# Optimization experiments

Hardware: AMD Instinct MI355X
Metric: run time of the kernel (lower is better)

Reference implementation:

```python
import jax, jax.numpy as jnp
import numpy as np

B, S, D, H, F = 16, 512, 768, 12, 3072
E = 4      # unique sequence-level experts
M = 4      # inner SwitchFeedForward experts
SW = 128   # switch encoder dim
EPS = 1e-12


def setup_inputs() -> dict:
    key = jax.random.key(0)
    ks = iter(jax.random.split(key, 64))
    def p(shape):
        return jax.random.normal(next(ks), shape, jnp.float32) * 0.02
    inp = {}
    inp['hidden_states'] = jax.random.normal(next(ks), (B, S, D), jnp.float32)
    inp['attention_mask'] = jnp.zeros((B, S), jnp.float32)
    inp['cluster_list'] = jnp.zeros((B,), jnp.int32)
    # router
    inp['sw_enc_w'] = p((D, SW)); inp['sw_enc_b'] = jnp.zeros((SW,), jnp.float32)
    inp['sw_w'] = p((SW, E));     inp['sw_b'] = jnp.zeros((E,), jnp.float32)
    # common attention
    for n in ('q', 'k', 'v', 'o'):
        inp['ca_w' + n] = p((D, D)); inp['ca_b' + n] = jnp.zeros((D,), jnp.float32)
    # unique attentions (stacked over E experts)
    for n in ('q', 'k', 'v', 'o'):
        inp['ua_w' + n] = p((E, D, D)); inp['ua_b' + n] = jnp.zeros((E, D), jnp.float32)
    # common FFN (plain GELU MLP)
    inp['cf_w1'] = p((D, F)); inp['cf_b1'] = jnp.zeros((F,), jnp.float32)
    inp['cf_w2'] = p((F, D)); inp['cf_b2'] = jnp.zeros((D,), jnp.float32)
    # unique FFNs: each is a top-1 SwitchFeedForward with M inner experts
    inp['uf_sw_w'] = p((E, D, M)); inp['uf_sw_b'] = jnp.zeros((E, M), jnp.float32)
    inp['uf_w1'] = p((E, M, D, F)); inp['uf_b1'] = jnp.zeros((E, M, F), jnp.float32)
    inp['uf_w2'] = p((E, M, F, D)); inp['uf_b2'] = jnp.zeros((E, M, D), jnp.float32)
    # output LayerNorm
    inp['ln_g'] = jnp.ones((D,), jnp.float32); inp['ln_b'] = jnp.zeros((D,), jnp.float32)
    return inp


def _attn(x, mask, wq, bq, wk, bk, wv, bv, wo, bo):
    b, s, d = x.shape
    dh = d // H
    q = (x @ wq + bq).reshape(b, s, H, dh)
    k = (x @ wk + bk).reshape(b, s, H, dh)
    v = (x @ wv + bv).reshape(b, s, H, dh)
    sc = jnp.einsum('bqhd,bkhd->bhqk', q, k) / jnp.sqrt(jnp.float32(dh))
    sc = sc + mask[:, None, None, :]
    pr = jax.nn.softmax(sc, axis=-1)
    o = jnp.einsum('bhqk,bkhd->bqhd', pr, v).reshape(b, s, d)
    return o @ wo + bo


def _switch_ffn(x, sww, swb, w1, b1, w2, b2):
    # top-1 token routing over M inner experts, output scaled by route_prob_max
    rp = jax.nn.softmax(x @ sww + swb, axis=-1)            # [b,s,M]
    gate = jax.nn.one_hot(jnp.argmax(rp, -1), M) * jnp.max(rp, -1, keepdims=True)
    h = jax.nn.gelu(jnp.einsum('bsd,mdf->bsmf', x, w1) + b1, approximate=False)
    y = jnp.einsum('bsmf,mfd->bsmd', h, w2) + b2
    return jnp.einsum('bsm,bsmd->bsd', gate, y)


def _forward(hidden_states, attention_mask, sw_enc_w, sw_enc_b, sw_w, sw_b,
             ca_wq, ca_bq, ca_wk, ca_bk, ca_wv, ca_bv, ca_wo, ca_bo,
             ua_wq, ua_bq, ua_wk, ua_bk, ua_wv, ua_bv, ua_wo, ua_bo,
             cf_w1, cf_b1, cf_w2, cf_b2,
             uf_sw_w, uf_sw_b, uf_w1, uf_b1, uf_w2, uf_b2, ln_g, ln_b):
    # sequence-level router: softmax over pooled hidden states, top-1 expert
    pooled = hidden_states.mean(axis=1)                    # [B,D]
    rp = jax.nn.softmax((pooled @ sw_enc_w + sw_enc_b) @ sw_w + sw_b, axis=-1)
    pm = jnp.max(rp, axis=-1)                              # [B]
    sel = jax.nn.one_hot(jnp.argmax(rp, axis=-1), E)       # [B,E]

    common_attn = _attn(hidden_states, attention_mask,
                        ca_wq, ca_bq, ca_wk, ca_bk, ca_wv, ca_bv, ca_wo, ca_bo)
    unique_attn = jnp.zeros_like(hidden_states)
    for i in range(E):
        oi = _attn(hidden_states, attention_mask,
                   ua_wq[i], ua_bq[i], ua_wk[i], ua_bk[i],
                   ua_wv[i], ua_bv[i], ua_wo[i], ua_bo[i])
        unique_attn = unique_attn + sel[:, i, None, None] * oi
    unique_attn = unique_attn * pm[:, None, None]          # scale by route prob
    att_output = common_attn + unique_attn

    unique_ffn = jnp.zeros_like(hidden_states)
    for i in range(E):
        yi = _switch_ffn(att_output, uf_sw_w[i], uf_sw_b[i],
                         uf_w1[i], uf_b1[i], uf_w2[i], uf_b2[i])
        unique_ffn = unique_ffn + sel[:, i, None, None] * yi
    common_ffn = jax.nn.gelu(att_output @ cf_w1 + cf_b1, approximate=False) @ cf_w2 + cf_b2
    ffn_output = common_ffn + unique_ffn                   # dropout is identity (eval)

    x = att_output + ffn_output
    mu = x.mean(-1, keepdims=True)
    var = jnp.mean((x - mu) ** 2, -1, keepdims=True)
    return (x - mu) / jnp.sqrt(var + EPS) * ln_g + ln_b


def reference(hidden_states, attention_mask, cluster_list, sw_enc_w, sw_enc_b, sw_w, sw_b,
              ca_wq, ca_bq, ca_wk, ca_bk, ca_wv, ca_bv, ca_wo, ca_bo,
              ua_wq, ua_bq, ua_wk, ua_bk, ua_wv, ua_bv, ua_wo, ua_bo,
              cf_w1, cf_b1, cf_w2, cf_b2,
              uf_sw_w, uf_sw_b, uf_w1, uf_b1, uf_w2, uf_b2, ln_g, ln_b):
    # cluster_list is only used in the warm-up branch; warm_up_step=0 -> ignored
    return _forward(hidden_states, attention_mask, sw_enc_w, sw_enc_b, sw_w, sw_b,
                    ca_wq, ca_bq, ca_wk, ca_bk, ca_wv, ca_bv, ca_wo, ca_bo,
                    ua_wq, ua_bq, ua_wk, ua_bk, ua_wv, ua_bv, ua_wo, ua_bo,
                    cf_w1, cf_b1, cf_w2, cf_b2,
                    uf_sw_w, uf_sw_b, uf_w1, uf_b1, uf_w2, uf_b2, ln_g, ln_b)
```

## Files before the change

kernel.cpp:

```cpp
#include <hip/hip_runtime.h>
#include <cstdint>
#include <cstddef>

#define Bq  16
#define Sq  512
#define Dq  768
#define Hq  12
#define DHq 64
#define Fq  3072
#define SWq 128
#define NTq 8192

typedef float        f32x4  __attribute__((ext_vector_type(4)));
typedef float        f32x16 __attribute__((ext_vector_type(16)));
typedef unsigned int u32x4  __attribute__((ext_vector_type(4)));
typedef __bf16       bf16x8 __attribute__((ext_vector_type(8)));
typedef _Float16     f16x8  __attribute__((ext_vector_type(8)));
typedef _Float16     f16x4  __attribute__((ext_vector_type(4)));
typedef _Float16     f16x2  __attribute__((ext_vector_type(2)));
typedef int          i32x2  __attribute__((ext_vector_type(2)));

__device__ __forceinline__ unsigned short f2bf(float f){
  unsigned int u = __builtin_bit_cast(unsigned int, f);
  u = (u + 0x7fffu + ((u >> 16) & 1u)) >> 16;
  return (unsigned short)u;
}
__device__ __forceinline__ unsigned int pk2(float a, float b){
  return (unsigned int)f2bf(a) | ((unsigned int)f2bf(b) << 16);
}
__device__ __forceinline__ i32x2 pl32swap(unsigned int a, unsigned int b){
  return __builtin_amdgcn_permlane32_swap((int)a, (int)b, false, false);
}
__device__ __forceinline__ f16x2 cvt_pk(float a, float b){
  return __builtin_bit_cast(f16x2, __builtin_amdgcn_cvt_pkrtz(a, b));
}

typedef __attribute__((address_space(1))) void vg_t;
typedef __attribute__((address_space(3))) void vl_t;
__device__ __forceinline__ void gl_lds16(const void* g, void* l){
  __builtin_amdgcn_global_load_lds((vg_t*)g, (vl_t*)l, 16, 0, 0);
}

__device__ __forceinline__ void swz2d(int &bx, int &by){
  const int gx = gridDim.x, gy = gridDim.y;
  const int nb = gx * gy;
  const int bid = blockIdx.y * gx + blockIdx.x;
  if (((nb & 7) == 0) && ((gy & 7) == 0)){
    const int chunk = nb >> 3;
    const int lb = (bid & 7) * chunk + (bid >> 3);
    const int bw = gx << 3;
    const int band = lb / bw;
    const int wn = lb - band * bw;
    bx = wn >> 3;
    by = (band << 3) + (wn & 7);
  } else {
    bx = blockIdx.x; by = blockIdx.y;
  }
}

__global__ void pooled_partial_k(const float* __restrict__ x, float* __restrict__ part){
  const int b = blockIdx.x, dc = blockIdx.y, z = blockIdx.z;
  const int d = dc*256 + threadIdx.x;
  const float* p = x + (size_t)b*Sq*Dq + (size_t)z*128*Dq + d;
  float s = 0.f;
  #pragma unroll 4
  for (int i = 0; i < 128; i++) s += p[(size_t)i*Dq];
  part[((size_t)z*Bq + b)*Dq + d] = s;
}

__global__ void router_seq_k(const float* __restrict__ part,
    const float* __restrict__ ew, const float* __restrict__ eb,
    const float* __restrict__ sw, const float* __restrict__ sb,
    int* __restrict__ sel, float* __restrict__ pm)
{
  const int b = blockIdx.x, j = threadIdx.x;
  __shared__ float h[SWq];
  __shared__ float pl[Dq];
  #pragma unroll
  for (int i = 0; i < 6; i++){
    int d = j + i*128;
    float s = part[(size_t)(0*Bq+b)*Dq + d] + part[(size_t)(1*Bq+b)*Dq + d]
            + part[(size_t)(2*Bq+b)*Dq + d] + part[(size_t)(3*Bq+b)*Dq + d];
    pl[d] = s * (1.0f/512.0f);
  }
  __syncthreads();
  float a = eb[j];
  for (int d = 0; d < Dq; d++) a += pl[d] * ew[d*SWq + j];
  h[j] = a;
  __syncthreads();
  if (j == 0){
    float lg[4];
    for (int e = 0; e < 4; e++){
      float t = sb[e];
      for (int k = 0; k < SWq; k++) t += h[k] * sw[k*4 + e];
      lg[e] = t;
    }
    float mx = fmaxf(fmaxf(lg[0],lg[1]), fmaxf(lg[2],lg[3]));
    float p[4], ssum = 0.f;
    for (int e = 0; e < 4; e++){ p[e] = expf(lg[e]-mx); ssum += p[e]; }
    int am = 0; float bv = p[0];
    for (int e = 1; e < 4; e++) if (p[e] > bv){ bv = p[e]; am = e; }
    sel[b] = am; pm[b] = bv/ssum;
  }
}

__global__ void split_f16_k(const float* __restrict__ x, _Float16* __restrict__ hh,
                            _Float16* __restrict__ ll, int n4){
  const int i = blockIdx.x*256 + threadIdx.x;
  if (i >= n4) return;
  f32x4 v = ((const f32x4*)x)[i];
  f16x4 vh, vl;
  #pragma unroll
  for (int j = 0; j < 4; j++){
    float s = v[j] * 1024.0f;
    _Float16 a = (_Float16)s;
    vh[j] = a;
    vl[j] = (_Float16)(s - (float)a);
  }
  ((f16x4*)hh)[i] = vh;
  ((f16x4*)ll)[i] = vl;
}

__global__ void transpose_f16s_k(const float* __restrict__ src,
    _Float16* __restrict__ dH, _Float16* __restrict__ dL,
    int K, int N, long srcStride, long dstStride, int rowOff)
{
  __shared__ float t[64][65];
  const int tid = threadIdx.x;
  const size_t so = (size_t)blockIdx.z * srcStride;
  const size_t dof = (size_t)blockIdx.z * dstStride;
  const int k0 = blockIdx.y * 64, n0 = blockIdx.x * 64;
  const int r = tid >> 2, c0 = (tid & 3) * 16;
  const float* sp = src + so + (size_t)(k0 + r) * N + n0 + c0;
  #pragma unroll
  for (int cc = 0; cc < 16; cc += 4){
    f32x4 v = *(const f32x4*)(sp + cc);
    t[r][c0+cc] = v[0]; t[r][c0+cc+1] = v[1]; t[r][c0+cc+2] = v[2]; t[r][c0+cc+3] = v[3];
  }
  __syncthreads();
  _Float16* ph = dH + dof + (size_t)(rowOff + n0 + r) * K + k0 + c0;
  _Float16* pl = dL + dof + (size_t)(rowOff + n0 + r) * K + k0 + c0;
  #pragma unroll
  for (int cc = 0; cc < 16; cc += 4){
    f16x4 vh, vl;
    #pragma unroll
    for (int j = 0; j < 4; j++){
      float s = t[c0+cc+j][r] * 1024.0f;
      _Float16 a = (_Float16)s;
      vh[j] = a; vl[j] = (_Float16)(s - (float)a);
    }
    *(f16x4*)(ph + cc) = vh;
    *(f16x4*)(pl + cc) = vl;
  }
}

__global__ void concat_bias3_k(const float* __restrict__ bq, const float* __restrict__ bk,
    const float* __restrict__ bv, float* __restrict__ dst, int srcStride)
{
  const int e = blockIdx.y;
  const int i = blockIdx.x*256 + threadIdx.x;
  dst[(size_t)e*2304 + i]        = bq[(size_t)e*srcStride + i];
  dst[(size_t)e*2304 + 768 + i]  = bk[(size_t)e*srcStride + i];
  dst[(size_t)e*2304 + 1536 + i] = bv[(size_t)e*srcStride + i];
}

template<int BMODE, int OMODE>
__global__ __launch_bounds__(256,2) void gemm_f16s_k(
    const _Float16* __restrict__ AH, const _Float16* __restrict__ AL,
    const _Float16* __restrict__ BH, const _Float16* __restrict__ BL,
    const float* __restrict__ bias, float* __restrict__ C,
    _Float16* __restrict__ Ch, _Float16* __restrict__ Cl,
    int N, int K, long estride, int bias_stride,
    const int* __restrict__ sel, const float* __restrict__ pm)
{
  __shared__ _Float16 AsH[128][32];
  __shared__ _Float16 AsL[128][32];
  __shared__ _Float16 BsH[128][32];
  __shared__ _Float16 BsL[128][32];
  const int tid = threadIdx.x;
  const int lane = tid & 63, wave = tid >> 6;
  const int wm = wave >> 1, wn = wave & 1;
  int bx, by; swz2d(bx, by);
  const int row0 = by * 128, col0 = bx * 128;
  const _Float16* bh = BH; const _Float16* bl = BL; const float* bp = bias;
  float cs = 1.0f;
  if constexpr (BMODE == 1){
    const int e = sel[row0 >> 9];
    bh += (size_t)e * estride; bl += (size_t)e * estride;
    bp += (size_t)e * bias_stride;
  }
  if constexpr (OMODE == 1) cs = pm[row0 >> 9];

  const int lr = lane >> 2, lk = (lane & 3) * 8;
  const _Float16 *pAH[2], *pAL[2], *pBH[2], *pBL[2];
  _Float16 *lAH[2], *lAL[2], *lBH[2], *lBL[2];
  #pragma unroll
  for (int j = 0; j < 2; j++){
    const int ia = wave*2 + j;
    pAH[j] = AH + (size_t)(row0 + ia*16 + lr)*K + lk;
    pAL[j] = AL + (size_t)(row0 + ia*16 + lr)*K + lk;
    pBH[j] = bh + (size_t)(col0 + ia*16 + lr)*K + lk;
    pBL[j] = bl + (size_t)(col0 + ia*16 + lr)*K + lk;
    lAH[j] = &AsH[0][0] + ia*512;
    lAL[j] = &AsL[0][0] + ia*512;
    lBH[j] = &BsH[0][0] + ia*512;
    lBL[j] = &BsL[0][0] + ia*512;
  }

  f32x4 acc[4][4];
  #pragma unroll
  for (int mi=0;mi<4;mi++)
    #pragma unroll
    for (int ni=0;ni<4;ni++) acc[mi][ni] = (f32x4){0.f,0.f,0.f,0.f};

  for (int k0 = 0; k0 < K; k0 += 32){
    __syncthreads();
    #pragma unroll
    for (int j = 0; j < 2; j++){
      gl_lds16(pAH[j] + k0, lAH[j]);
      gl_lds16(pAL[j] + k0, lAL[j]);
      gl_lds16(pBH[j] + k0, lBH[j]);
      gl_lds16(pBL[j] + k0, lBL[j]);
    }
    __syncthreads();
    f16x8 fah[4], fal[4], fbh[4], fbl[4];
    #pragma unroll
    for (int mi=0;mi<4;mi++){
      const int r = wm*64 + mi*16 + (lane&15), c = 8*(lane>>4);
      fah[mi] = __builtin_bit_cast(f16x8, *(const u32x4*)&AsH[r][c]);
      fal[mi] = __builtin_bit_cast(f16x8, *(const u32x4*)&AsL[r][c]);
    }
    #pragma unroll
    for (int ni=0;ni<4;ni++){
      const int r = wn*64 + ni*16 + (lane&15), c = 8*(lane>>4);
      fbh[ni] = __builtin_bit_cast(f16x8, *(const u32x4*)&BsH[r][c]);
      fbl[ni] = __builtin_bit_cast(f16x8, *(const u32x4*)&BsL[r][c]);
    }
    #pragma unroll
    for (int mi=0;mi<4;mi++)
      #pragma unroll
      for (int ni=0;ni<4;ni++){
        acc[mi][ni] = __builtin_amdgcn_mfma_f32_16x16x32_f16(fah[mi], fbh[ni], acc[mi][ni], 0, 0, 0);
        acc[mi][ni] = __builtin_amdgcn_mfma_f32_16x16x32_f16(fah[mi], fbl[ni], acc[mi][ni], 0, 0, 0);
        acc[mi][ni] = __builtin_amdgcn_mfma_f32_16x16x32_f16(fal[mi], fbh[ni], acc[mi][ni], 0, 0, 0);
      }
  }

  const float INV = 1.0f/1048576.0f;
  const int erow = 4*(lane >> 4);
  const int ecol = lane & 15;
  #pragma unroll
  for (int mi=0;mi<4;mi++)
    #pragma unroll
    for (int ni=0;ni<4;ni++){
      const int c = col0 + wn*64 + ni*16 + ecol;
      const float bb = bp[c];
      #pragma unroll
      for (int r=0;r<4;r++){
        const int R = row0 + wm*64 + mi*16 + erow + r;
        const float v = acc[mi][ni][r]*INV + bb;
        if constexpr (OMODE == 0){
          C[(size_t)R*N + c] = v;
        } else if constexpr (OMODE == 1){
          C[(size_t)R*N + c] += cs*v;
        } else {
          const float vs = v * 1024.0f;
          const _Float16 hi = (_Float16)vs;
          Ch[(size_t)R*N + c] = hi;
          Cl[(size_t)R*N + c] = (_Float16)(vs - (float)hi);
        }
      }
    }
}

__global__ __launch_bounds__(256,2) void attn_mfma_k(
    const _Float16* __restrict__ qkvH, const _Float16* __restrict__ qkvL,
    const float* __restrict__ mask,
    _Float16* __restrict__ ctxH, _Float16* __restrict__ ctxL)
{
  __shared__ _Float16 Kh[64][72], Kl[64][72];
  __shared__ _Float16 Vh[64][72], Vl[64][72];
  __shared__ float msk[64];
  __shared__ float rsi[4][32];
  const int qb = blockIdx.x, h = blockIdx.y, b = blockIdx.z;
  const int tid = threadIdx.x;
  const int l = tid & 63, w = tid >> 6;
  const int l31 = l & 31, g5 = l >> 5;
  const float SC = 1.0f/8388608.0f;

  u32x4 qfh[4], qfl[4];
  {
    const size_t qoff = (size_t)(b*Sq + qb*128 + w*32 + l31) * 2304 + h*DHq + g5*8;
    #pragma unroll
    for (int c = 0; c < 4; c++){
      qfh[c] = *(const u32x4*)(qkvH + qoff + c*16);
      qfl[c] = *(const u32x4*)(qkvL + qoff + c*16);
    }
  }
  f32x16 oacc[2];
  #pragma unroll
  for (int nt = 0; nt < 2; nt++)
    #pragma unroll
    for (int i = 0; i < 16; i++) oacc[nt][i] = 0.f;
  float rsl = 0.f;
  const float* mrow = mask + b*Sq;

  for (int kt = 0; kt < 8; kt++){
    __syncthreads();
    {
      const size_t krow = (size_t)(b*Sq + kt*64 + l) * 2304 + 768 + h*DHq;
      #pragma unroll
      for (int i = 0; i < 2; i++){
        const int ch = w + i*4;
        *(u32x4*)&Kh[l][ch*8] = *(const u32x4*)(qkvH + krow + ch*8);
        *(u32x4*)&Kl[l][ch*8] = *(const u32x4*)(qkvL + krow + ch*8);
      }
      const size_t vrow = krow + 768 + w*16;
      f16x8 v0 = __builtin_bit_cast(f16x8, *(const u32x4*)(qkvH + vrow));
      f16x8 v1 = __builtin_bit_cast(f16x8, *(const u32x4*)(qkvH + vrow + 8));
      f16x8 u0 = __builtin_bit_cast(f16x8, *(const u32x4*)(qkvL + vrow));
      f16x8 u1 = __builtin_bit_cast(f16x8, *(const u32x4*)(qkvL + vrow + 8));
      #pragma unroll
      for (int i = 0; i < 8; i++){
        Vh[w*16 + i][l] = v0[i]; Vh[w*16 + 8 + i][l] = v1[i];
        Vl[w*16 + i][l] = u0[i]; Vl[w*16 + 8 + i][l] = u1[i];
      }
      if (tid < 64) msk[tid] = mrow[kt*64 + tid] + 6.9314718055994531f;
    }
    __syncthreads();

    f32x16 sacc[2];
    #pragma unroll
    for (int mt = 0; mt < 2; mt++)
      #pragma unroll
      for (int i = 0; i < 16; i++) sacc[mt][i] = 0.f;
    #pragma unroll
    for (int mt = 0; mt < 2; mt++){
      #pragma unroll
      for (int c = 0; c < 4; c++){
        f16x8 kh = __builtin_bit_cast(f16x8, *(const u32x4*)&Kh[mt*32 + l31][c*16 + g5*8]);
        f16x8 kl = __builtin_bit_cast(f16x8, *(const u32x4*)&Kl[mt*32 + l31][c*16 + g5*8]);
        f16x8 qh = __builtin_bit_cast(f16x8, qfh[c]);
        f16x8 ql = __builtin_bit_cast(f16x8, qfl[c]);
        sacc[mt] = __builtin_amdgcn_mfma_f32_32x32x16_f16(kh, qh, sacc[mt], 0, 0, 0);
        sacc[mt] = __builtin_amdgcn_mfma_f32_32x32x16_f16(kh, ql, sacc[mt], 0, 0, 0);
        sacc[mt] = __builtin_amdgcn_mfma_f32_32x32x16_f16(kl, qh, sacc[mt], 0, 0, 0);
      }
    }

    unsigned int hP[2][4][2], lP[2][4][2];
    #pragma unroll
    for (int mt = 0; mt < 2; mt++){
      #pragma unroll
      for (int m = 0; m < 4; m++){
        f32x4 mk = *(const f32x4*)&msk[mt*32 + m*8 + g5*4];
        float p0 = __expf(fmaf(sacc[mt][4*m+0], SC, mk[0]));
        float p1 = __expf(fmaf(sacc[mt][4*m+1], SC, mk[1]));
        float p2 = __expf(fmaf(sacc[mt][4*m+2], SC, mk[2]));
        float p3 = __expf(fmaf(sacc[mt][4*m+3], SC, mk[3]));
        rsl += (p0 + p1) + (p2 + p3);
        f16x2 h0 = cvt_pk(p0, p1);
        f16x2 h1 = cvt_pk(p2, p3);
        f16x2 e0, e1;
        e0[0] = (_Float16)(p0 - (float)h0[0]); e0[1] = (_Float16)(p1 - (float)h0[1]);
        e1[0] = (_Float16)(p2 - (float)h1[0]); e1[1] = (_Float16)(p3 - (float)h1[1]);
        hP[mt][m][0] = __builtin_bit_cast(unsigned int, h0);
        hP[mt][m][1] = __builtin_bit_cast(unsigned int, h1);
        lP[mt][m][0] = __builtin_bit_cast(unsigned int, e0);
        lP[mt][m][1] = __builtin_bit_cast(unsigned int, e1);
      }
    }

    #pragma unroll
    for (int mt = 0; mt < 2; mt++){
      #pragma unroll
      for (int cc = 0; cc < 2; cc++){
        i32x2 sh0 = pl32swap(hP[mt][2*cc][0], hP[mt][2*cc+1][0]);
        i32x2 sh1 = pl32swap(hP[mt][2*cc][1], hP[mt][2*cc+1][1]);
        i32x2 sl0 = pl32swap(lP[mt][2*cc][0], lP[mt][2*cc+1][0]);
        i32x2 sl1 = pl32swap(lP[mt][2*cc][1], lP[mt][2*cc+1][1]);
        u32x4 pah = (u32x4){(unsigned)sh0[0], (unsigned)sh1[0], (unsigned)sh0[1], (unsigned)sh1[1]};
        u32x4 pal = (u32x4){(unsigned)sl0[0], (unsigned)sl1[0], (unsigned)sl0[1], (unsigned)sl1[1]};
        f16x8 ph = __builtin_bit_cast(f16x8, pah);
        f16x8 pe = __builtin_bit_cast(f16x8, pal);
        const int kof = (mt*2 + cc)*16 + g5*8;
        #pragma unroll
        for (int nt = 0; nt < 2; nt++){
          f16x8 vh = __builtin_bit_cast(f16x8, *(const u32x4*)&Vh[nt*32 + l31][kof]);
          f16x8 vl = __builtin_bit_cast(f16x8, *(const u32x4*)&Vl[nt*32 + l31][kof]);
          oacc[nt] = __builtin_amdgcn_mfma_f32_32x32x16_f16(ph, vh, oacc[nt], 0, 0, 0);
          oacc[nt] = __builtin_amdgcn_mfma_f32_32x32x16_f16(ph, vl, oacc[nt], 0, 0, 0);
          oacc[nt] = __builtin_amdgcn_mfma_f32_32x32x16_f16(pe, vh, oacc[nt], 0, 0, 0);
        }
      }
    }
  }

  {
    unsigned int rb = __builtin_bit_cast(unsigned int, rsl);
    i32x2 sw = pl32swap(rb, rb);
    float partner = __builtin_bit_cast(float, (l >= 32) ? sw[0] : sw[1]);
    float tot = rsl + partner;
    if (l < 32) rsi[w][l31] = 1.0f / tot;
  }
  __syncthreads();

  const size_t obase = (size_t)(b*Sq + qb*128 + w*32);
  #pragma unroll
  for (int nt = 0; nt < 2; nt++){
    const int col = h*DHq + nt*32 + l31;
    #pragma unroll
    for (int r = 0; r < 16; r++){
      const int q = (r&3) + 8*(r>>2) + 4*g5;
      const float v = oacc[nt][r] * rsi[w][q];
      const _Float16 hi = (_Float16)v;
      const size_t off = (obase + q)*Dq + col;
      ctxH[off] = hi;
      ctxL[off] = (_Float16)(v - (float)hi);
    }
  }
}

__global__ void transpose_bf16_k(const float* __restrict__ src, unsigned short* __restrict__ dst,
                                 int K, int N)
{
  __shared__ float t[64][65];
  const int tid = threadIdx.x;
  const size_t mo = (size_t)blockIdx.z * K * N;
  const int k0 = blockIdx.y * 64, n0 = blockIdx.x * 64;
  const int r = tid >> 2, c0 = (tid & 3) * 16;
  const float* sp = src + mo + (size_t)(k0 + r) * N + n0 + c0;
  #pragma unroll
  for (int cc = 0; cc < 16; cc += 4){
    f32x4 v = *(const f32x4*)(sp + cc);
    t[r][c0+cc] = v[0]; t[r][c0+cc+1] = v[1]; t[r][c0+cc+2] = v[2]; t[r][c0+cc+3] = v[3];
  }
  __syncthreads();
  unsigned short* dp = dst + mo + (size_t)(n0 + r) * K + k0 + c0;
  u32x4 h0, h1v;
  #pragma unroll
  for (int i = 0; i < 4; i++) h0[i]  = pk2(t[c0+2*i  ][r], t[c0+2*i+1][r]);
  #pragma unroll
  for (int i = 0; i < 4; i++) h1v[i] = pk2(t[c0+8+2*i][r], t[c0+9+2*i][r]);
  *(u32x4*)(dp)     = h0;
  *(u32x4*)(dp + 8) = h1v;
}

template<int MT, int AMODE, int OMODE, bool GELU_, bool GROUPED>
__global__ __launch_bounds__(256,2) void gemm_bf16_k(
    const void* __restrict__ Av, const unsigned short* __restrict__ BT,
    const float* __restrict__ bias, float* __restrict__ Cf, unsigned short* __restrict__ Cb,
    int N, int K,
    const int* __restrict__ tile_g, const int* __restrict__ tile_r0,
    const int* __restrict__ grp_off, const int* __restrict__ n_tiles,
    const int* __restrict__ tok_idx, const float* __restrict__ gate_s,
    size_t bstride, int bias_stride)
{
  constexpr int MI = MT / 32;
  constexpr int AI = MT / 64;
  __shared__ unsigned short As[MT][32];
  __shared__ unsigned short Bs[128][32];
  const int tid = threadIdx.x;
  const int lane = tid & 63, wave = tid >> 6;
  const int wm = wave >> 1, wn = wave & 1;
  int col0, row0, gend = 1 << 30, g = 0;
  if constexpr (GROUPED){
    const int gx = gridDim.x;
    const int nb = gx * gridDim.y;
    const int bid = blockIdx.y * gx + blockIdx.x;
    int lb = bid;
    if ((nb & 7) == 0) lb = (bid & 7) * (nb >> 3) + (bid >> 3);
    const int t = lb / gx;
    col0 = (lb - t * gx) * 128;
    if (t >= *n_tiles) return;
    g = tile_g[t];
    row0 = grp_off[g] + tile_r0[t];
    gend = grp_off[g+1];
  } else {
    int bx, by; swz2d(bx, by);
    row0 = by * MT;
    col0 = bx * 128;
  }
  const unsigned short* Bp = BT + (size_t)g * bstride;
  const float* bp = bias + (size_t)g * bias_stride;

  const int lr = lane >> 2, lk8 = (lane & 3) * 8;
  const unsigned short* pB[2]; unsigned short* lB[2];
  #pragma unroll
  for (int j = 0; j < 2; j++){
    const int ib = wave*2 + j;
    pB[j] = Bp + (size_t)(col0 + ib*16 + lr)*K + lk8;
    lB[j] = &Bs[0][0] + ib*512;
  }
  const unsigned short* pA2[AI]; unsigned short* lA2[AI];
  const float* afp = nullptr; int sa_r = 0, sa_k = 0;
  if constexpr (AMODE == 2){
    #pragma unroll
    for (int j = 0; j < AI; j++){
      int r = row0 + (wave*AI + j)*16 + lr;
      if constexpr (GROUPED) r = (r < gend - 1) ? r : (gend - 1);
      pA2[j] = (const unsigned short*)Av + (size_t)r*K + lk8;
      lA2[j] = &As[0][0] + (wave*AI + j)*512;
    }
  } else {
    sa_r = (MT == 128) ? (tid >> 1) : (tid >> 2);
    sa_k = (MT == 128) ? ((tid & 1) * 16) : ((tid & 3) * 8);
    int arow = row0 + sa_r;
    if constexpr (GROUPED) arow = (arow < gend - 1) ? arow : (gend - 1);
    if constexpr (AMODE == 1) arow = tok_idx[arow];
    afp = (const float*)Av + (size_t)arow * K + sa_k;
  }

  f32x4 acc[MI][4];
  #pragma unroll
  for (int mi=0;mi<MI;mi++)
    #pragma unroll
    for (int ni=0;ni<4;ni++) acc[mi][ni] = (f32x4){0.f,0.f,0.f,0.f};

  for (int k0 = 0; k0 < K; k0 += 32){
    u32x4 al0, al1;
    if constexpr (AMODE != 2){
      f32x4 f0 = *(const f32x4*)(afp + k0);
      f32x4 f1 = *(const f32x4*)(afp + k0 + 4);
      al0[0]=pk2(f0[0],f0[1]); al0[1]=pk2(f0[2],f0[3]); al0[2]=pk2(f1[0],f1[1]); al0[3]=pk2(f1[2],f1[3]);
      if constexpr (MT == 128){
        f32x4 f2 = *(const f32x4*)(afp + k0 + 8);
        f32x4 f3 = *(const f32x4*)(afp + k0 + 12);
        al1[0]=pk2(f2[0],f2[1]); al1[1]=pk2(f2[2],f2[3]); al1[2]=pk2(f3[0],f3[1]); al1[3]=pk2(f3[2],f3[3]);
      }
    }
    __syncthreads();
    if constexpr (AMODE == 2){
      #pragma unroll
      for (int j = 0; j < AI; j++) gl_lds16(pA2[j] + k0, lA2[j]);
    } else {
      *(u32x4*)&As[sa_r][sa_k] = al0;
      if constexpr (MT == 128) *(u32x4*)&As[sa_r][sa_k + 8] = al1;
    }
    gl_lds16(pB[0] + k0, lB[0]);
    gl_lds16(pB[1] + k0, lB[1]);
    __syncthreads();
    bf16x8 af[MI], bfr[4];
    #pragma unroll
    for (int mi=0;mi<MI;mi++){
      u32x4 t = *(const u32x4*)&As[wm*(MT/2) + mi*16 + (lane&15)][8*(lane>>4)];
      af[mi] = __builtin_bit_cast(bf16x8, t);
    }
    #pragma unroll
    for (int ni=0;ni<4;ni++){
      u32x4 t = *(const u32x4*)&Bs[wn*64 + ni*16 + (lane&15)][8*(lane>>4)];
      bfr[ni] = __builtin_bit_cast(bf16x8, t);
    }
    #pragma unroll
    for (int mi=0;mi<MI;mi++)
      #pragma unroll
      for (int ni=0;ni<4;ni++)
        acc[mi][ni] = __builtin_amdgcn_mfma_f32_16x16x32_bf16(af[mi], bfr[ni], acc[mi][ni], 0, 0, 0);
  }

  const int erow = 4*(lane >> 4);
  const int ecol = lane & 15;
  #pragma unroll
  for (int mi=0;mi<MI;mi++)
    #pragma unroll
    for (int ni=0;ni<4;ni++){
      const int c = col0 + wn*64 + ni*16 + ecol;
      const float bb = bp[c];
      #pragma unroll
      for (int r=0;r<4;r++){
        const int R = row0 + wm*(MT/2) + mi*16 + erow + r;
        if (GROUPED && R >= gend) continue;
        float v = acc[mi][ni][r] + bb;
        if (GELU_) v = 0.5f*v*(1.0f + erff(v*0.70710678118654752f));
        if constexpr (OMODE == 0){
          Cb[(size_t)R*N + c] = f2bf(v);
        } else if constexpr (OMODE == 1){
          Cf[(size_t)R*N + c] = v;
        } else {
          const int tok = tok_idx[R];
          const float gt = gate_s[R];
          float* p = Cf + (size_t)tok*N + c;
          *p += gt*v;
        }
      }
    }
}

__global__ void token_router_k(const float* __restrict__ att, const int* __restrict__ sel,
    const float* __restrict__ sww, const float* __restrict__ swb,
    int* __restrict__ grp, float* __restrict__ gate, int* __restrict__ grp_cnt)
{
  const int t = blockIdx.x*4 + (threadIdx.x >> 6);
  const int lane = threadIdx.x & 63;
  const int e = sel[t >> 9];
  const float* x = att + (size_t)t * Dq;
  const float* w = sww + (size_t)e * Dq * 4;
  float a0=0.f, a1=0.f, a2=0.f, a3=0.f;
  #pragma unroll 4
  for (int i = 0; i < 12; i++){
    const int d = lane + i*64;
    const float xv = x[d];
    f32x4 wv = *(const f32x4*)&w[d*4];
    a0 += xv*wv[0]; a1 += xv*wv[1]; a2 += xv*wv[2]; a3 += xv*wv[3];
  }
  #pragma unroll
  for (int off = 32; off; off >>= 1){
    a0 += __shfl_xor(a0, off); a1 += __shfl_xor(a1, off);
    a2 += __shfl_xor(a2, off); a3 += __shfl_xor(a3, off);
  }
  if (lane == 0){
    const float l0 = a0 + swb[e*4+0], l1 = a1 + swb[e*4+1];
    const float l2 = a2 + swb[e*4+2], l3 = a3 + swb[e*4+3];
    const float mx = fmaxf(fmaxf(l0,l1), fmaxf(l2,l3));
    const float p0 = expf(l0-mx), p1 = expf(l1-mx), p2 = expf(l2-mx), p3 = expf(l3-mx);
    const float ssum = p0+p1+p2+p3;
    int am = 0; float bv = p0;
    if (p1 > bv){ bv=p1; am=1; }
    if (p2 > bv){ bv=p2; am=2; }
    if (p3 > bv){ bv=p3; am=3; }
    grp[t] = e*4 + am;
    gate[t] = bv/ssum;
    atomicAdd(&grp_cnt[e*4 + am], 1);
  }
}

__global__ void build_offsets_k(const int* __restrict__ grp_cnt, int* __restrict__ grp_off,
    int* __restrict__ tg128, int* __restrict__ tr128, int* __restrict__ nt128,
    int* __restrict__ tg64, int* __restrict__ tr64, int* __restrict__ nt64)
{
  int off = 0, n1 = 0, n2 = 0;
  for (int g = 0; g < 16; g++){
    grp_off[g] = off;
    const int c = grp_cnt[g];
    for (int r0 = 0; r0 < c; r0 += 128){ tg128[n1] = g; tr128[n1] = r0; n1++; }
    for (int r0 = 0; r0 < c; r0 += 64){  tg64[n2]  = g; tr64[n2]  = r0; n2++; }
    off += c;
  }
  grp_off[16] = off;
  *nt128 = n1; *nt64 = n2;
}

__global__ void scatter_k(const int* __restrict__ grp, const float* __restrict__ gate,
    const int* __restrict__ grp_off, int* __restrict__ fill,
    int* __restrict__ tok_idx, float* __restrict__ gate_s)
{
  const int t = blockIdx.x*256 + threadIdx.x;
  const int g = grp[t];
  const int pos = grp_off[g] + atomicAdd(&fill[g], 1);
  tok_idx[pos] = t;
  gate_s[pos] = gate[t];
}

__global__ __launch_bounds__(256) void final_ln_k(const float* __restrict__ att,
    const float* __restrict__ acc, const float* __restrict__ lg,
    const float* __restrict__ lb, float* __restrict__ out)
{
  const int row = blockIdx.x, tid = threadIdx.x;
  const float* a = att + (size_t)row * Dq;
  const float* c = acc + (size_t)row * Dq;
  float x[3];
  #pragma unroll
  for (int i = 0; i < 3; i++) x[i] = a[tid + 256*i] + c[tid + 256*i];
  __shared__ float red[256];
  red[tid] = x[0] + x[1] + x[2];
  __syncthreads();
  for (int st = 128; st; st >>= 1){
    if (tid < st) red[tid] += red[tid + st];
    __syncthreads();
  }
  const float mu = red[0] * (1.0f/768.0f);
  __syncthreads();
  const float d0 = x[0]-mu, d1 = x[1]-mu, d2 = x[2]-mu;
  red[tid] = d0*d0 + d1*d1 + d2*d2;
  __syncthreads();
  for (int st = 128; st; st >>= 1){
    if (tid < st) red[tid] += red[tid + st];
    __syncthreads();
  }
  const float inv = 1.0f/sqrtf(red[0]*(1.0f/768.0f) + 1e-12f);
  #pragma unroll
  for (int i = 0; i < 3; i++){
    const int col = tid + 256*i;
    out[(size_t)row*Dq + col] = (x[i]-mu)*inv*lg[col] + lb[col];
  }
}

extern "C" void kernel_launch(void* const* d_in, const int* in_sizes, int n_in,
                              void* d_out, int out_size, void* d_ws, size_t ws_size,
                              hipStream_t stream)
{
  (void)in_sizes; (void)n_in; (void)out_size; (void)ws_size;
  const float* hs    = (const float*)d_in[0];
  const float* amask = (const float*)d_in[1];
  const float* sw_enc_w = (const float*)d_in[3];
  const float* sw_enc_b = (const float*)d_in[4];
  const float* sw_w  = (const float*)d_in[5];
  const float* sw_b  = (const float*)d_in[6];
  const float* ca_wq = (const float*)d_in[7];
  const float* ca_bq = (const float*)d_in[8];
  const float* ca_wk = (const float*)d_in[9];
  const float* ca_bk = (const float*)d_in[10];
  const float* ca_wv = (const float*)d_in[11];
  const float* ca_bv = (const float*)d_in[12];
  const float* ca_wo = (const float*)d_in[13];
  const float* ca_bo = (const float*)d_in[14];
  const float* ua_wq = (const float*)d_in[15];
  const float* ua_bq = (const float*)d_in[16];
  const float* ua_wk = (const float*)d_in[17];
  const float* ua_bk = (const float*)d_in[18];
  const float* ua_wv = (const float*)d_in[19];
  const float* ua_bv = (const float*)d_in[20];
  const float* ua_wo = (const float*)d_in[21];
  const float* ua_bo = (const float*)d_in[22];
  const float* cf_w1 = (const float*)d_in[23];
  const float* cf_b1 = (const float*)d_in[24];
  const float* cf_w2 = (const float*)d_in[25];
  const float* cf_b2 = (const float*)d_in[26];
  const float* uf_sw_w = (const float*)d_in[27];
  const float* uf_sw_b = (const float*)d_in[28];
  const float* uf_w1 = (const float*)d_in[29];
  const float* uf_b1 = (const float*)d_in[30];
  const float* uf_w2 = (const float*)d_in[31];
  const float* uf_b2 = (const float*)d_in[32];
  const float* ln_g  = (const float*)d_in[33];
  const float* ln_b  = (const float*)d_in[34];
  float* out = (float*)d_out;

  char* W = (char*)d_ws;
  int*   sel     = (int*)(W + 0);
  float* pm      = (float*)(W + 64);
  int*   grp_cnt = (int*)(W + 128);
  int*   fill    = (int*)(W + 192);
  int*   ntile   = (int*)(W + 256);
  int*   ntile64 = (int*)(W + 320);
  int*   grp_off = (int*)(W + 512);
  int*   tile_g  = (int*)(W + 1024);
  int*   tile_r  = (int*)(W + 2048);
  int*   tile_g64= (int*)(W + 3072);
  int*   tile_r64= (int*)(W + 4096);

  float* att  = (float*)(W + 8192);
  float* facc = (float*)(W + 25174016);
  const size_t X = 50339840;
  _Float16* hsH  = (_Float16*)(W + X);
  _Float16* hsL  = (_Float16*)(W + X + 12582912);
  _Float16* qkvH = (_Float16*)(W + X + 25165824);
  _Float16* qkvL = (_Float16*)(W + X + 62914560);
  _Float16* ctxH = (_Float16*)(W + X + 100663296);
  _Float16* ctxL = (_Float16*)(W + X + 113246208);
  _Float16* wqkv_cH = (_Float16*)(W + X + 125829120);
  _Float16* wqkv_cL = (_Float16*)(W + X + 129368064);
  _Float16* wqkv_uH = (_Float16*)(W + X + 132907008);
  _Float16* wqkv_uL = (_Float16*)(W + X + 147062784);
  _Float16* wo_cH   = (_Float16*)(W + X + 161218560);
  _Float16* wo_cL   = (_Float16*)(W + X + 162398208);
  _Float16* wo_uH   = (_Float16*)(W + X + 163577856);
  _Float16* wo_uL   = (_Float16*)(W + X + 168296448);
  float* qkvb_c = (float*)(W + X + 173015040);
  float* qkvb_u = (float*)(W + X + 173024256);
  float* partb  = (float*)(W + X + 173061120);

  unsigned short* w1T = (unsigned short*)(W + X);
  unsigned short* w2T = (unsigned short*)(W + X + 80216064);
  unsigned short* h1  = (unsigned short*)(W + X + 160432128);
  int*   grp     = (int*)(W + 261103616);
  float* gate    = (float*)(W + 261136384);
  int*   tok_idx = (int*)(W + 261169152);
  float* gate_s  = (float*)(W + 261201920);

  hipMemsetAsync(W, 0, 512, stream);

  pooled_partial_k<<<dim3(Bq,3,4),256,0,stream>>>(hs, partb);
  router_seq_k<<<Bq,128,0,stream>>>(partb, sw_enc_w, sw_enc_b, sw_w, sw_b, sel, pm);

  split_f16_k<<<6144,256,0,stream>>>(hs, hsH, hsL, NTq*Dq/4);
  transpose_f16s_k<<<dim3(12,12,1),256,0,stream>>>(ca_wq, wqkv_cH, wqkv_cL, Dq, Dq, 0, 0, 0);
  transpose_f16s_k<<<dim3(12,12,1),256,0,stream>>>(ca_wk, wqkv_cH, wqkv_cL, Dq, Dq, 0, 0, 768);
  transpose_f16s_k<<<dim3(12,12,1),256,0,stream>>>(ca_wv, wqkv_cH, wqkv_cL, Dq, Dq, 0, 0, 1536);
  transpose_f16s_k<<<dim3(12,12,4),256,0,stream>>>(ua_wq, wqkv_uH, wqkv_uL, Dq, Dq, (long)Dq*Dq, (long)2304*768, 0);
  transpose_f16s_k<<<dim3(12,12,4),256,0,stream>>>(ua_wk, wqkv_uH, wqkv_uL, Dq, Dq, (long)Dq*Dq, (long)2304*768, 768);
  transpose_f16s_k<<<dim3(12,12,4),256,0,stream>>>(ua_wv, wqkv_uH, wqkv_uL, Dq, Dq, (long)Dq*Dq, (long)2304*768, 1536);
  transpose_f16s_k<<<dim3(12,12,1),256,0,stream>>>(ca_wo, wo_cH, wo_cL, Dq, Dq, 0, 0, 0);
  transpose_f16s_k<<<dim3(12,12,4),256,0,stream>>>(ua_wo, wo_uH, wo_uL, Dq, Dq, (long)Dq*Dq, (long)Dq*Dq, 0);
  concat_bias3_k<<<dim3(3,1),256,0,stream>>>(ca_bq, ca_bk, ca_bv, qkvb_c, 0);
  concat_bias3_k<<<dim3(3,4),256,0,stream>>>(ua_bq, ua_bk, ua_bv, qkvb_u, 768);

  gemm_f16s_k<0,2><<<dim3(18,64),256,0,stream>>>(hsH, hsL, wqkv_cH, wqkv_cL, qkvb_c,
      nullptr, qkvH, qkvL, 2304, Dq, 0, 0, nullptr, nullptr);
  attn_mfma_k<<<dim3(4,Hq,Bq),256,0,stream>>>(qkvH, qkvL, amask, ctxH, ctxL);
  gemm_f16s_k<0,0><<<dim3(6,64),256,0,stream>>>(ctxH, ctxL, wo_cH, wo_cL, ca_bo,
      att, nullptr, nullptr, Dq, Dq, 0, 0, nullptr, nullptr);

  gemm_f16s_k<1,2><<<dim3(18,64),256,0,stream>>>(hsH, hsL, wqkv_uH, wqkv_uL, qkvb_u,
      nullptr, qkvH, qkvL, 2304, Dq, (long)2304*768, 2304, sel, nullptr);
  attn_mfma_k<<<dim3(4,Hq,Bq),256,0,stream>>>(qkvH, qkvL, amask, ctxH, ctxL);
  gemm_f16s_k<1,1><<<dim3(6,64),256,0,stream>>>(ctxH, ctxL, wo_uH, wo_uL, ua_bo,
      att, nullptr, nullptr, Dq, Dq, (long)Dq*Dq, Dq, sel, pm);

  transpose_bf16_k<<<dim3(48,12,1), 256,0,stream>>>(cf_w1, w1T, Dq, Fq);
  transpose_bf16_k<<<dim3(48,12,16),256,0,stream>>>(uf_w1, w1T + 2359296, Dq, Fq);
  transpose_bf16_k<<<dim3(12,48,1), 256,0,stream>>>(cf_w2, w2T, Fq, Dq);
  transpose_bf16_k<<<dim3(12,48,16),256,0,stream>>>(uf_w2, w2T + 2359296, Fq, Dq);

  gemm_bf16_k<128,0,0,true,false><<<dim3(24,64),256,0,stream>>>((const void*)att, w1T, cf_b1, nullptr, h1,
      Fq, Dq, nullptr,nullptr,nullptr,nullptr,nullptr,nullptr, (size_t)0, 0);
  gemm_bf16_k<64,2,1,false,false><<<dim3(6,128),256,0,stream>>>((const void*)h1, w2T, cf_b2, facc, nullptr,
      Dq, Fq, nullptr,nullptr,nullptr,nullptr,nullptr,nullptr, (size_t)0, 0);

  token_router_k<<<2048,256,0,stream>>>(att, sel, uf_sw_w, uf_sw_b, grp, gate, grp_cnt);
  build_offsets_k<<<1,1,0,stream>>>(grp_cnt, grp_off, tile_g, tile_r, ntile, tile_g64, tile_r64, ntile64);
  scatter_k<<<32,256,0,stream>>>(grp, gate, grp_off, fill, tok_idx, gate_s);

  gemm_bf16_k<128,1,0,true,true><<<dim3(24,80),256,0,stream>>>((const void*)att, w1T + 2359296, uf_b1, nullptr, h1,
      Fq, Dq, tile_g, tile_r, grp_off, ntile, tok_idx, gate_s, (size_t)2359296, Fq);
  gemm_bf16_k<64,2,2,false,true><<<dim3(6,144),256,0,stream>>>((const void*)h1, w2T + 2359296, uf_b2, facc, nullptr,
      Dq, Fq, tile_g64, tile_r64, grp_off, ntile64, tok_idx, gate_s, (size_t)2359296, Dq);

  final_ln_k<<<NTq,256,0,stream>>>(att, facc, ln_g, ln_b, out);
}
```

Measured before the change: 1.151 ms.

## Double-buffer LDS tiles in f16-split and bf16 GEMM kernels

Both GEMM kernels now keep two LDS stages for the A and B tiles. The next K-slice is issued into the alternate buffer before the MFMA work on the current one, which leaves one barrier per iteration instead of two. In the bf16 kernel, the fp32 A loads are moved ahead of the MFMAs and their bf16 conversion and LDS store after them. The aim is to hide global-load latency behind matrix math, at the cost of doubled LDS use (64KB per block in the f16 kernel), which may limit occupancy, and extra live registers.

```diff
diff --git a/kernel.cpp b/kernel.cpp
--- a/kernel.cpp
+++ b/kernel.cpp
@@ -173,10 +173,10 @@
     int N, int K, long estride, int bias_stride,
     const int* __restrict__ sel, const float* __restrict__ pm)
 {
-  __shared__ _Float16 AsH[128][32];
-  __shared__ _Float16 AsL[128][32];
-  __shared__ _Float16 BsH[128][32];
-  __shared__ _Float16 BsL[128][32];
+  __shared__ _Float16 AsH[2][128][32];
+  __shared__ _Float16 AsL[2][128][32];
+  __shared__ _Float16 BsH[2][128][32];
+  __shared__ _Float16 BsL[2][128][32];
   const int tid = threadIdx.x;
   const int lane = tid & 63, wave = tid >> 6;
   const int wm = wave >> 1, wn = wave & 1;
@@ -193,7 +193,6 @@
 
   const int lr = lane >> 2, lk = (lane & 3) * 8;
   const _Float16 *pAH[2], *pAL[2], *pBH[2], *pBL[2];
-  _Float16 *lAH[2], *lAL[2], *lBH[2], *lBL[2];
   #pragma unroll
   for (int j = 0; j < 2; j++){
     const int ia = wave*2 + j;
@@ -201,11 +200,17 @@
     pAL[j] = AL + (size_t)(row0 + ia*16 + lr)*K + lk;
     pBH[j] = bh + (size_t)(col0 + ia*16 + lr)*K + lk;
     pBL[j] = bl + (size_t)(col0 + ia*16 + lr)*K + lk;
-    lAH[j] = &AsH[0][0] + ia*512;
-    lAL[j] = &AsL[0][0] + ia*512;
-    lBH[j] = &BsH[0][0] + ia*512;
-    lBL[j] = &BsL[0][0] + ia*512;
-  }
+  }
+  auto stage = [&](int c, int kk){
+    #pragma unroll
+    for (int j = 0; j < 2; j++){
+      const int ia = wave*2 + j;
+      gl_lds16(pAH[j] + kk, &AsH[0][0][0] + c*4096 + ia*512);
+      gl_lds16(pAL[j] + kk, &AsL[0][0][0] + c*4096 + ia*512);
+      gl_lds16(pBH[j] + kk, &BsH[0][0][0] + c*4096 + ia*512);
+      gl_lds16(pBL[j] + kk, &BsL[0][0][0] + c*4096 + ia*512);
+    }
+  };
 
   f32x4 acc[4][4];
   #pragma unroll
@@ -213,28 +218,23 @@
     #pragma unroll
     for (int ni=0;ni<4;ni++) acc[mi][ni] = (f32x4){0.f,0.f,0.f,0.f};
 
+  stage(0, 0);
+  int cur = 0;
   for (int k0 = 0; k0 < K; k0 += 32){
     __syncthreads();
-    #pragma unroll
-    for (int j = 0; j < 2; j++){
-      gl_lds16(pAH[j] + k0, lAH[j]);
-      gl_lds16(pAL[j] + k0, lAL[j]);
-      gl_lds16(pBH[j] + k0, lBH[j]);
-      gl_lds16(pBL[j] + k0, lBL[j]);
-    }
-    __syncthreads();
+    if (k0 + 32 < K) stage(cur ^ 1, k0 + 32);
     f16x8 fah[4], fal[4], fbh[4], fbl[4];
     #pragma unroll
     for (int mi=0;mi<4;mi++){
       const int r = wm*64 + mi*16 + (lane&15), c = 8*(lane>>4);
-      fah[mi] = __builtin_bit_cast(f16x8, *(const u32x4*)&AsH[r][c]);
-      fal[mi] = __builtin_bit_cast(f16x8, *(const u32x4*)&AsL[r][c]);
+      fah[mi] = __builtin_bit_cast(f16x8, *(const u32x4*)&AsH[cur][r][c]);
+      fal[mi] = __builtin_bit_cast(f16x8, *(const u32x4*)&AsL[cur][r][c]);
     }
     #pragma unroll
     for (int ni=0;ni<4;ni++){
       const int r = wn*64 + ni*16 + (lane&15), c = 8*(lane>>4);
-      fbh[ni] = __builtin_bit_cast(f16x8, *(const u32x4*)&BsH[r][c]);
-      fbl[ni] = __builtin_bit_cast(f16x8, *(const u32x4*)&BsL[r][c]);
+      fbh[ni] = __builtin_bit_cast(f16x8, *(const u32x4*)&BsH[cur][r][c]);
+      fbl[ni] = __builtin_bit_cast(f16x8, *(const u32x4*)&BsL[cur][r][c]);
     }
     #pragma unroll
     for (int mi=0;mi<4;mi++)
@@ -244,6 +244,7 @@
         acc[mi][ni] = __builtin_amdgcn_mfma_f32_16x16x32_f16(fah[mi], fbl[ni], acc[mi][ni], 0, 0, 0);
         acc[mi][ni] = __builtin_amdgcn_mfma_f32_16x16x32_f16(fal[mi], fbh[ni], acc[mi][ni], 0, 0, 0);
       }
+    cur ^= 1;
   }
 
   const float INV = 1.0f/1048576.0f;
@@ -458,8 +459,8 @@
 {
   constexpr int MI = MT / 32;
   constexpr int AI = MT / 64;
-  __shared__ unsigned short As[MT][32];
-  __shared__ unsigned short Bs[128][32];
+  __shared__ unsigned short As[2][MT][32];
+  __shared__ unsigned short Bs[2][128][32];
   const int tid = threadIdx.x;
   const int lane = tid & 63, wave = tid >> 6;
   const int wm = wave >> 1, wn = wave & 1;
@@ -485,14 +486,17 @@
   const float* bp = bias + (size_t)g * bias_stride;
 
   const int lr = lane >> 2, lk8 = (lane & 3) * 8;
-  const unsigned short* pB[2]; unsigned short* lB[2];
+  const unsigned short* pB[2];
   #pragma unroll
   for (int j = 0; j < 2; j++){
     const int ib = wave*2 + j;
     pB[j] = Bp + (size_t)(col0 + ib*16 + lr)*K + lk8;
-    lB[j] = &Bs[0][0] + ib*512;
-  }
-  const unsigned short* pA2[AI]; unsigned short* lA2[AI];
+  }
+  auto stageB = [&](int c, int kk){
+    gl_lds16(pB[0] + kk, &Bs[0][0][0] + c*4096 + (wave*2+0)*512);
+    gl_lds16(pB[1] + kk, &Bs[0][0][0] + c*4096 + (wave*2+1)*512);
+  };
+  const unsigned short* pA2[AI];
   const float* afp = nullptr; int sa_r = 0, sa_k = 0;
   if constexpr (AMODE == 2){
     #pragma unroll
@@ -500,7 +504,6 @@
       int r = row0 + (wave*AI + j)*16 + lr;
       if constexpr (GROUPED) r = (r < gend - 1) ? r : (gend - 1);
       pA2[j] = (const unsigned short*)Av + (size_t)r*K + lk8;
-      lA2[j] = &As[0][0] + (wave*AI + j)*512;
     }
   } else {
     sa_r = (MT == 128) ? (tid >> 1) : (tid >> 2);
@@ -510,6 +513,11 @@
     if constexpr (AMODE == 1) arow = tok_idx[arow];
     afp = (const float*)Av + (size_t)arow * K + sa_k;
   }
+  auto stageA2 = [&](int c, int kk){
+    #pragma unroll
+    for (int j = 0; j < AI; j++)
+      gl_lds16(pA2[j] + kk, &As[0][0][0] + c*(MT*32) + (wave*AI + j)*512);
+  };
 
   f32x4 acc[MI][4];
   #pragma unroll
@@ -517,45 +525,73 @@
     #pragma unroll
     for (int ni=0;ni<4;ni++) acc[mi][ni] = (f32x4){0.f,0.f,0.f,0.f};
 
-  for (int k0 = 0; k0 < K; k0 += 32){
-    u32x4 al0, al1;
-    if constexpr (AMODE != 2){
-      f32x4 f0 = *(const f32x4*)(afp + k0);
-      f32x4 f1 = *(const f32x4*)(afp + k0 + 4);
-      al0[0]=pk2(f0[0],f0[1]); al0[1]=pk2(f0[2],f0[3]); al0[2]=pk2(f1[0],f1[1]); al0[3]=pk2(f1[2],f1[3]);
-      if constexpr (MT == 128){
-        f32x4 f2 = *(const f32x4*)(afp + k0 + 8);
-        f32x4 f3 = *(const f32x4*)(afp + k0 + 12);
-        al1[0]=pk2(f2[0],f2[1]); al1[1]=pk2(f2[2],f2[3]); al1[2]=pk2(f3[0],f3[1]); al1[3]=pk2(f3[2],f3[3]);
-      }
-    }
+  const int nt = K >> 5;
+  if constexpr (AMODE == 2){
+    stageA2(0, 0);
+  } else {
+    f32x4 f0 = *(const f32x4*)(afp);
+    f32x4 f1 = *(const f32x4*)(afp + 4);
+    u32x4 al0;
+    al0[0]=pk2(f0[0],f0[1]); al0[1]=pk2(f0[2],f0[3]); al0[2]=pk2(f1[0],f1[1]); al0[3]=pk2(f1[2],f1[3]);
+    *(u32x4*)&As[0][sa_r][sa_k] = al0;
+    if constexpr (MT == 128){
+      f32x4 f2 = *(const f32x4*)(afp + 8);
+      f32x4 f3 = *(const f32x4*)(afp + 12);
+      u32x4 al1;
+      al1[0]=pk2(f2[0],f2[1]); al1[1]=pk2(f2[2],f2[3]); al1[2]=pk2(f3[0],f3[1]); al1[3]=pk2(f3[2],f3[3]);
+      *(u32x4*)&As[0][sa_r][sa_k + 8] = al1;
+    }
+  }
+  stageB(0, 0);
+
+  int cur = 0;
+  for (int t = 0; t < nt; t++){
     __syncthreads();
-    if constexpr (AMODE == 2){
-      #pragma unroll
-      for (int j = 0; j < AI; j++) gl_lds16(pA2[j] + k0, lA2[j]);
-    } else {
-      *(u32x4*)&As[sa_r][sa_k] = al0;
-      if constexpr (MT == 128) *(u32x4*)&As[sa_r][sa_k + 8] = al1;
-    }
-    gl_lds16(pB[0] + k0, lB[0]);
-    gl_lds16(pB[1] + k0, lB[1]);
-    __syncthreads();
+    const int k1 = (t + 1) << 5;
+    f32x4 f0n, f1n, f2n, f3n;
+    const bool nxt = (t + 1 < nt);
+    if (nxt){
+      if constexpr (AMODE == 2){
+        stageA2(cur ^ 1, k1);
+      } else {
+        f0n = *(const f32x4*)(afp + k1);
+        f1n = *(const f32x4*)(afp + k1 + 4);
+        if constexpr (MT == 128){
+          f2n = *(const f32x4*)(afp + k1 + 8);
+          f3n = *(const f32x4*)(afp + k1 + 12);
+        }
+      }
+      stageB(cur ^ 1, k1);
+    }
     bf16x8 af[MI], bfr[4];
     #pragma unroll
     for (int mi=0;mi<MI;mi++){
-      u32x4 t = *(const u32x4*)&As[wm*(MT/2) + mi*16 + (lane&15)][8*(lane>>4)];
-      af[mi] = __builtin_bit_cast(bf16x8, t);
+      u32x4 tt = *(const u32x4*)&As[cur][wm*(MT/2) + mi*16 + (lane&15)][8*(lane>>4)];
+      af[mi] = __builtin_bit_cast(bf16x8, tt);
     }
     #pragma unroll
     for (int ni=0;ni<4;ni++){
-      u32x4 t = *(const u32x4*)&Bs[wn*64 + ni*16 + (lane&15)][8*(lane>>4)];
-      bfr[ni] = __builtin_bit_cast(bf16x8, t);
+      u32x4 tt = *(const u32x4*)&Bs[cur][wn*64 + ni*16 + (lane&15)][8*(lane>>4)];
+      bfr[ni] = __builtin_bit_cast(bf16x8, tt);
     }
     #pragma unroll
     for (int mi=0;mi<MI;mi++)
       #pragma unroll
       for (int ni=0;ni<4;ni++)
         acc[mi][ni] = __builtin_amdgcn_mfma_f32_16x16x32_bf16(af[mi], bfr[ni], acc[mi][ni], 0, 0, 0);
+    if (nxt){
+      if constexpr (AMODE != 2){
+        u32x4 al0;
+        al0[0]=pk2(f0n[0],f0n[1]); al0[1]=pk2(f0n[2],f0n[3]); al0[2]=pk2(f1n[0],f1n[1]); al0[3]=pk2(f1n[2],f1n[3]);
+        *(u32x4*)&As[cur^1][sa_r][sa_k] = al0;
+        if constexpr (MT == 128){
+          u32x4 al1;
+          al1[0]=pk2(f2n[0],f2n[1]); al1[1]=pk2(f2n[2],f2n[3]); al1[2]=pk2(f3n[0],f3n[1]); al1[3]=pk2(f3n[2],f3n[3]);
+          *(u32x4*)&As[cur^1][sa_r][sa_k + 8] = al1;
+        }
+      }
+    }
+    cur ^= 1;
   }
 
   const int erow = 4*(lane >> 4);
```

New measurement: 1.174 ms. Within noise of the previous version (+2.0%).
